# Kernel optimization log

Hardware: AMD Instinct MI355X
Metric: run time of the kernel (lower is better)

## Reference

```python
import jax, jax.numpy as jnp
import numpy as np

B, S, D, H, DK, DV, SEG = 2, 4096, 1024, 8, 128, 128, 512
NSEG = S // SEG


def setup_inputs() -> dict:
    key = jax.random.key(0)
    k0, k1, k2, k3, k4, k5 = jax.random.split(key, 6)
    return {
        "x": jax.random.normal(k0, (B, S, D), jnp.float32),
        "Wk": jax.random.normal(k1, (H, D, DK), jnp.float32) / np.float32(np.sqrt(D)),
        "Wv": jax.random.normal(k2, (H, D, DV), jnp.float32) / np.float32(np.sqrt(D)),
        "Wq": jax.random.normal(k3, (H, D, DK), jnp.float32) / np.float32(np.sqrt(D)),
        "Wout": jax.random.normal(k4, (H * DV, D), jnp.float32) / np.float32(np.sqrt(H * DV)),
        "betas": jax.random.normal(k5, (1, H, 1, DV), jnp.float32),
    }


def reference(x, Wk, Wv, Wq, Wout, betas):
    # Per-head projections: (B,H,S,dk/dv)
    k_full = jnp.einsum('bsd,hdk->bhsk', x, Wk)
    v_full = jnp.einsum('bsd,hdk->bhsk', x, Wv)
    q_full = jnp.einsum('bsd,hdk->bhsk', x, Wq)

    def to_segs(t):  # (B,H,S,E) -> (NSEG,B,H,SEG,E)
        return t.reshape(B, H, NSEG, SEG, t.shape[-1]).transpose(2, 0, 1, 3, 4)

    segs = (to_segs(k_full), to_segs(v_full), to_segs(q_full))

    mem0 = jnp.zeros((B, H, DK, DV), x.dtype)           # compressive memory
    z0 = jnp.full((B, H, DK, 1), 1.0 / DK, x.dtype)     # normalizer
    causal_mask = jnp.tril(jnp.ones((SEG, SEG), bool))
    gate = jax.nn.sigmoid(betas)                        # (1,H,1,DV)
    scale = jnp.asarray(1.0 / np.sqrt(DK), x.dtype)

    def step(carry, seg):
        mem, z = carry
        k, v, q = seg                                   # (B,H,SEG,dk/dv)
        sigma_q = jax.nn.elu(q) + 1.0
        # segment-local causal softmax attention
        scores = jnp.einsum('bhik,bhjk->bhij', q, k) * scale
        scores = jnp.where(causal_mask, scores, -jnp.inf)
        att_dot = jax.nn.softmax(scores, axis=-1) @ v
        # linear-attention read from memory
        att_mem = (sigma_q @ mem) / (sigma_q @ z)
        # delta-rule memory update
        sigma_k = jax.nn.elu(k) + 1.0
        mem = mem + jnp.einsum('bhsk,bhsv->bhkv', sigma_k, v - (sigma_k @ mem) / (sigma_k @ z))
        z = z + jnp.sum(sigma_k, axis=-2, keepdims=True).swapaxes(-1, -2)
        # gated mix of memory and local attention
        att = gate * att_mem + (1.0 - gate) * att_dot   # (B,H,SEG,DV)
        att = att.transpose(0, 2, 1, 3).reshape(B, SEG, H * DV)
        return (mem, z), att @ Wout                     # (B,SEG,D)

    _, outs = jax.lax.scan(step, (mem0, z0), segs)      # (NSEG,B,SEG,D)
    return outs.transpose(1, 0, 2, 3).reshape(B, S, D)
```

## Files before the change

### kernel.cpp

```cpp
#include <hip/hip_runtime.h>

#define B_  2
#define S_  4096
#define D_  1024
#define H_  8
#define DK_ 128
#define DV_ 128
#define SEG_ 512
#define NSEG_ 8
#define BH_ 16
#define M_ 8192

typedef __attribute__((ext_vector_type(8))) short bf16x8;
typedef __attribute__((ext_vector_type(4))) float f32x4;

__device__ __forceinline__ float elu1(float x) { return x > 0.f ? x + 1.f : __expf(x); }
__device__ __forceinline__ float sigmoidf(float x) { return 1.f / (1.f + __expf(-x)); }

__device__ __forceinline__ unsigned short f2b(float f) {
    union { float f; unsigned int u; } x; x.f = f;
    unsigned int r = x.u + 0x7fffu + ((x.u >> 16) & 1u);
    return (unsigned short)(r >> 16);
}
__device__ __forceinline__ float b2f(unsigned short u) {
    union { unsigned int u; float f; } x; x.u = ((unsigned int)u) << 16; return x.f;
}

__device__ __forceinline__ void gl2lds16(const void* g, void* l) {
    __builtin_amdgcn_global_load_lds(
        (const __attribute__((address_space(1))) void*)g,
        (__attribute__((address_space(3))) void*)l, 16, 0, 0);
}

__global__ __launch_bounds__(256) void conv_bf16(
    const float* __restrict__ src, unsigned short* __restrict__ dst)
{
    int i = (blockIdx.x * 256 + threadIdx.x) * 4;
    float4 v = *(const float4*)(src + i);
    ushort4 o;
    o.x = f2b(v.x); o.y = f2b(v.y); o.z = f2b(v.z); o.w = f2b(v.w);
    *(ushort4*)(dst + i) = o;
}

__global__ __launch_bounds__(256) void transpose_conv(
    const float* __restrict__ src, unsigned short* __restrict__ dst, int R, int C)
{
    __shared__ float tile[32][33];
    const size_t moff = (size_t)blockIdx.z * R * C;
    src += moff; dst += moff;
    const int c0 = blockIdx.x * 32, r0 = blockIdx.y * 32;
    const int tx = threadIdx.x & 31, ty = threadIdx.x >> 5;
    #pragma unroll
    for (int i = 0; i < 32; i += 8)
        tile[ty + i][tx] = src[(size_t)(r0 + ty + i) * C + c0 + tx];
    __syncthreads();
    #pragma unroll
    for (int i = 0; i < 32; i += 8)
        dst[(size_t)(c0 + ty + i) * R + r0 + tx] = f2b(tile[tx][ty + i]);
}

__global__ __launch_bounds__(256) void transpose_conv3(
    const float* __restrict__ Wk, const float* __restrict__ Wv,
    const float* __restrict__ Wq, unsigned short* __restrict__ dst)
{
    __shared__ float tile[32][33];
    const int z = blockIdx.z;
    const int w = z >> 3;
    const float* src = (w == 0) ? Wk : (w == 1) ? Wv : Wq;
    src += (size_t)(z & 7) * 131072;
    dst += (size_t)z * 131072;
    const int c0 = blockIdx.x * 32, r0 = blockIdx.y * 32;
    const int tx = threadIdx.x & 31, ty = threadIdx.x >> 5;
    #pragma unroll
    for (int i = 0; i < 32; i += 8)
        tile[ty + i][tx] = src[(size_t)(r0 + ty + i) * 128 + c0 + tx];
    __syncthreads();
    #pragma unroll
    for (int i = 0; i < 32; i += 8)
        dst[(size_t)(c0 + ty + i) * 1024 + r0 + tx] = f2b(tile[tx][ty + i]);
}

__global__ __launch_bounds__(256) void colsum_k(
    const unsigned short* __restrict__ Kbb, float* __restrict__ colsum)
{
    __shared__ float red[32][128];
    const int t = threadIdx.x;
    const int bh = blockIdx.x >> 3, seg = blockIdx.x & 7;
    const unsigned short* Kp = Kbb + ((size_t)bh * 4096 + seg * 512) * 128;
    const int rbase = t >> 3, c0 = (t & 7) * 16;
    float part[16] = {};
    for (int chunk = 0; chunk < 16; ++chunk) {
        const unsigned short* p = Kp + (size_t)(chunk * 32 + rbase) * 128 + c0;
        bf16x8 a = *(const bf16x8*)p;
        bf16x8 b = *(const bf16x8*)(p + 8);
        #pragma unroll
        for (int j = 0; j < 8; ++j) {
            part[j]     += elu1(b2f((unsigned short)a[j]));
            part[j + 8] += elu1(b2f((unsigned short)b[j]));
        }
    }
    #pragma unroll
    for (int j = 0; j < 16; ++j) red[rbase][c0 + j] = part[j];
    __syncthreads();
    if (t < 128) {
        float s = 0.f;
        #pragma unroll
        for (int r = 0; r < 32; ++r) s += red[r][t];
        colsum[(size_t)blockIdx.x * 128 + t] = s;
    }
}

__global__ __launch_bounds__(256) void den_z(
    const unsigned short* __restrict__ Kbb, const float* __restrict__ colsum,
    float* __restrict__ den, float* __restrict__ zseg)
{
    __shared__ float zs[128];
    const int t = threadIdx.x;
    const int bh = blockIdx.x >> 3, seg = blockIdx.x & 7;
    if (t < 128) {
        float z = 1.f / 128.f;
        for (int j = 0; j < seg; ++j) z += colsum[(size_t)(bh * 8 + j) * 128 + t];
        zs[t] = z;
        zseg[(size_t)blockIdx.x * 128 + t] = z;
    }
    __syncthreads();
    #pragma unroll
    for (int rr = 0; rr < 2; ++rr) {
        int s = t + rr * 256;
        const unsigned short* kp = Kbb + ((size_t)bh * 4096 + seg * 512 + s) * 128;
        float d = 0.f;
        #pragma unroll 4
        for (int f = 0; f < 16; ++f) {
            bf16x8 a = *(const bf16x8*)(kp + f * 8);
            #pragma unroll
            for (int j = 0; j < 8; ++j)
                d += elu1(b2f((unsigned short)a[j])) * zs[f * 8 + j];
        }
        den[(size_t)bh * 4096 + seg * 512 + s] = d;
    }
}

__global__ __launch_bounds__(256) void sigma_kT2(
    const unsigned short* __restrict__ Kbb, const float* __restrict__ den,
    unsigned short* __restrict__ SkT, unsigned short* __restrict__ SkTs)
{
    __shared__ float tile[32][33];
    __shared__ float rden[32];
    const int bh = blockIdx.z;
    const int s0 = blockIdx.x * 32, dk0 = blockIdx.y * 32;
    const int tx = threadIdx.x & 31, ty = threadIdx.x >> 5;
    if (threadIdx.x < 32) rden[threadIdx.x] = 1.f / den[(size_t)bh * 4096 + s0 + threadIdx.x];
    #pragma unroll
    for (int i = 0; i < 32; i += 8)
        tile[ty + i][tx] = elu1(b2f(Kbb[((size_t)bh * 4096 + s0 + ty + i) * 128 + dk0 + tx]));
    __syncthreads();
    #pragma unroll
    for (int i = 0; i < 32; i += 8) {
        float v = tile[tx][ty + i];
        size_t o = ((size_t)bh * 128 + dk0 + ty + i) * 4096 + s0 + tx;
        SkT[o]  = f2b(v);
        SkTs[o] = f2b(v * rden[tx]);
    }
}

__device__ __forceinline__ void mfma_gemm_128(
    const unsigned short* __restrict__ A, int lda,
    const unsigned short* __restrict__ Bt, int ldb, int K,
    unsigned short* As, unsigned short* Bs, f32x4 acc[4][4])
{
    const int tid = threadIdx.x;
    const int wave = tid >> 6, lane = tid & 63;
    const int r4 = lane >> 2;
    const int c4s = (((lane & 3) ^ ((lane >> 2) & 3)) * 8);
    const int lrow = lane & 15, lquad = lane >> 4;
    const int sl8 = (lquad ^ (lrow & 3)) * 8;
    const int wm = (wave >> 1) * 64, wn = (wave & 1) * 64;
    const int ar0 = wave * 32, ar1 = wave * 32 + 16;
    const int T = K >> 5;

    auto STAGE = [&](int t, int bufidx) {
        unsigned short* Ab = As + bufidx * 4096;
        unsigned short* Bb = Bs + bufidx * 4096;
        const int kk = t * 32;
        gl2lds16(A  + (size_t)(ar0 + r4) * lda + kk + c4s, Ab + ar0 * 32);
        gl2lds16(A  + (size_t)(ar1 + r4) * lda + kk + c4s, Ab + ar1 * 32);
        gl2lds16(Bt + (size_t)(ar0 + r4) * ldb + kk + c4s, Bb + ar0 * 32);
        gl2lds16(Bt + (size_t)(ar1 + r4) * ldb + kk + c4s, Bb + ar1 * 32);
    };

    STAGE(0, 0);
    STAGE(1, 1);
    int cur = 0;
    for (int t = 0; t < T; ++t) {
        if (t + 2 < T) {
            int nb = cur + 2; if (nb >= 3) nb -= 3;
            STAGE(t + 2, nb);
            asm volatile("s_waitcnt vmcnt(8)" ::: "memory");
        } else if (t + 1 < T) {
            asm volatile("s_waitcnt vmcnt(4)" ::: "memory");
        } else {
            asm volatile("s_waitcnt vmcnt(0)" ::: "memory");
        }
        __builtin_amdgcn_s_barrier();
        __builtin_amdgcn_sched_barrier(0);
        const unsigned short* Ac = As + cur * 4096;
        const unsigned short* Bc = Bs + cur * 4096;
        bf16x8 af[4], bfr[4];
        #pragma unroll
        for (int i = 0; i < 4; ++i)
            af[i] = *(const bf16x8*)(Ac + (wm + i * 16 + lrow) * 32 + sl8);
        #pragma unroll
        for (int j = 0; j < 4; ++j)
            bfr[j] = *(const bf16x8*)(Bc + (wn + j * 16 + lrow) * 32 + sl8);
        #pragma unroll
        for (int i = 0; i < 4; ++i)
            #pragma unroll
            for (int j = 0; j < 4; ++j)
                acc[i][j] = __builtin_amdgcn_mfma_f32_16x16x32_bf16(af[i], bfr[j], acc[i][j], 0, 0, 0);
        __builtin_amdgcn_s_barrier();
        __builtin_amdgcn_sched_barrier(0);
        cur += 1; if (cur >= 3) cur -= 3;
    }
}

__global__ __launch_bounds__(256) void gemm_qkv_mfma(
    const unsigned short* __restrict__ xb, const unsigned short* __restrict__ Wtb,
    unsigned short* __restrict__ Qbb, unsigned short* __restrict__ Kbb,
    unsigned short* __restrict__ Vtb)
{
    __shared__ unsigned short As[3 * 128 * 32];
    __shared__ unsigned short Bs[3 * 128 * 32];
    const int m0 = blockIdx.x * 128;
    const int panel = blockIdx.y;
    const int which = panel >> 3, h = panel & 7;
    f32x4 acc[4][4] = {};
    mfma_gemm_128(xb + (size_t)m0 * 1024, 1024,
                  Wtb + (size_t)panel * 128 * 1024, 1024, 1024, As, Bs, acc);
    const int tid = threadIdx.x, wave = tid >> 6, lane = tid & 63;
    const int lrow = lane & 15, lquad = lane >> 4;
    const int wm = (wave >> 1) * 64, wn = (wave & 1) * 64;
    if (which == 1) {
        #pragma unroll
        for (int i = 0; i < 4; ++i) {
            int mb = m0 + wm + i * 16 + lquad * 4;
            int bb = mb >> 12, sb = mb & 4095;
            int bh = bb * 8 + h;
            size_t vbase = ((size_t)bh * 8 + (sb >> 9)) * 128;
            #pragma unroll
            for (int j = 0; j < 4; ++j) {
                int col = wn + j * 16 + lrow;
                ushort4 o;
                o.x = f2b(acc[i][j][0]); o.y = f2b(acc[i][j][1]);
                o.z = f2b(acc[i][j][2]); o.w = f2b(acc[i][j][3]);
                *(ushort4*)(Vtb + ((vbase + col) * 512 + (sb & 511))) = o;
            }
        }
    } else {
        unsigned short* Dst = (which == 0) ? Kbb : Qbb;
        #pragma unroll
        for (int i = 0; i < 4; ++i)
            #pragma unroll
            for (int r = 0; r < 4; ++r) {
                int m = m0 + wm + i * 16 + lquad * 4 + r;
                int bb = m >> 12, s = m & 4095;
                int bh = bb * 8 + h;
                size_t rowbase = ((size_t)bh * 4096 + s) * 128;
                #pragma unroll
                for (int j = 0; j < 4; ++j)
                    Dst[rowbase + wn + j * 16 + lrow] = f2b(acc[i][j][r]);
            }
    }
}

__global__ __launch_bounds__(256) void gemm_out_mfma(
    const unsigned short* __restrict__ A, const unsigned short* __restrict__ Bt,
    float* __restrict__ C)
{
    __shared__ unsigned short As[3 * 128 * 32];
    __shared__ unsigned short Bs[3 * 128 * 32];
    const int m0 = blockIdx.x * 128, n0 = blockIdx.y * 128;
    f32x4 acc[4][4] = {};
    mfma_gemm_128(A + (size_t)m0 * 1024, 1024,
                  Bt + (size_t)n0 * 1024, 1024, 1024, As, Bs, acc);
    const int tid = threadIdx.x, wave = tid >> 6, lane = tid & 63;
    const int lrow = lane & 15, lquad = lane >> 4;
    const int wm = (wave >> 1) * 64, wn = (wave & 1) * 64;
    #pragma unroll
    for (int i = 0; i < 4; ++i)
        #pragma unroll
        for (int r = 0; r < 4; ++r) {
            int m = m0 + wm + i * 16 + lquad * 4 + r;
            #pragma unroll
            for (int j = 0; j < 4; ++j)
                C[(size_t)m * 1024 + n0 + wn + j * 16 + lrow] = acc[i][j][r];
        }
}

__global__ __launch_bounds__(256) void ac_gemm(
    const unsigned short* __restrict__ SkT, const unsigned short* __restrict__ SkTs,
    const unsigned short* __restrict__ Vtb,
    unsigned short* __restrict__ Emat, float* __restrict__ Cmat)
{
    __shared__ unsigned short As [3 * 128 * 32];
    __shared__ unsigned short Bs1[3 * 128 * 32];
    __shared__ unsigned short Bs2[3 * 128 * 32];
    const int bh = blockIdx.x >> 3, seg = blockIdx.x & 7;
    const unsigned short* Ap  = SkT  + (size_t)bh * 128 * 4096 + seg * 512;
    const unsigned short* B1p = SkTs + (size_t)bh * 128 * 4096 + seg * 512;
    const unsigned short* B2p = Vtb  + (size_t)blockIdx.x * 128 * 512;
    const int tid = threadIdx.x;
    const int wave = tid >> 6, lane = tid & 63;
    const int r4 = lane >> 2;
    const int c4s = (((lane & 3) ^ ((lane >> 2) & 3)) * 8);
    const int lrow = lane & 15, lquad = lane >> 4;
    const int sl8 = (lquad ^ (lrow & 3)) * 8;
    const int wm = (wave >> 1) * 64, wn = (wave & 1) * 64;
    const int ar0 = wave * 32, ar1 = wave * 32 + 16;
    f32x4 e[4][4] = {}, c[4][4] = {};

    auto STAGE = [&](int t, int bufidx) {
        unsigned short* Ab  = As  + bufidx * 4096;
        unsigned short* B1b = Bs1 + bufidx * 4096;
        unsigned short* B2b = Bs2 + bufidx * 4096;
        const int kk = t * 32;
        gl2lds16(Ap  + (size_t)(ar0 + r4) * 4096 + kk + c4s, Ab  + ar0 * 32);
        gl2lds16(Ap  + (size_t)(ar1 + r4) * 4096 + kk + c4s, Ab  + ar1 * 32);
        gl2lds16(B1p + (size_t)(ar0 + r4) * 4096 + kk + c4s, B1b + ar0 * 32);
        gl2lds16(B1p + (size_t)(ar1 + r4) * 4096 + kk + c4s, B1b + ar1 * 32);
        gl2lds16(B2p + (size_t)(ar0 + r4) * 512  + kk + c4s, B2b + ar0 * 32);
        gl2lds16(B2p + (size_t)(ar1 + r4) * 512  + kk + c4s, B2b + ar1 * 32);
    };

    STAGE(0, 0);
    STAGE(1, 1);
    int cur = 0;
    for (int t = 0; t < 16; ++t) {
        if (t + 2 < 16) {
            int nb = cur + 2; if (nb >= 3) nb -= 3;
            STAGE(t + 2, nb);
            asm volatile("s_waitcnt vmcnt(12)" ::: "memory");
        } else if (t + 1 < 16) {
            asm volatile("s_waitcnt vmcnt(6)" ::: "memory");
        } else {
            asm volatile("s_waitcnt vmcnt(0)" ::: "memory");
        }
        __builtin_amdgcn_s_barrier();
        __builtin_amdgcn_sched_barrier(0);
        const unsigned short* Ac  = As  + cur * 4096;
        const unsigned short* B1c = Bs1 + cur * 4096;
        const unsigned short* B2c = Bs2 + cur * 4096;
        bf16x8 af[4], b1[4], b2[4];
        #pragma unroll
        for (int i = 0; i < 4; ++i)
            af[i] = *(const bf16x8*)(Ac + (wm + i * 16 + lrow) * 32 + sl8);
        #pragma unroll
        for (int j = 0; j < 4; ++j) {
            b1[j] = *(const bf16x8*)(B1c + (wn + j * 16 + lrow) * 32 + sl8);
            b2[j] = *(const bf16x8*)(B2c + (wn + j * 16 + lrow) * 32 + sl8);
        }
        #pragma unroll
        for (int i = 0; i < 4; ++i)
            #pragma unroll
            for (int j = 0; j < 4; ++j) {
                e[i][j] = __builtin_amdgcn_mfma_f32_16x16x32_bf16(af[i], b1[j], e[i][j], 0, 0, 0);
                c[i][j] = __builtin_amdgcn_mfma_f32_16x16x32_bf16(af[i], b2[j], c[i][j], 0, 0, 0);
            }
        __builtin_amdgcn_s_barrier();
        __builtin_amdgcn_sched_barrier(0);
        cur += 1; if (cur >= 3) cur -= 3;
    }
    #pragma unroll
    for (int i = 0; i < 4; ++i)
        #pragma unroll
        for (int r = 0; r < 4; ++r) {
            int m = wm + i * 16 + lquad * 4 + r;
            #pragma unroll
            for (int j = 0; j < 4; ++j) {
                int nn = wn + j * 16 + lrow;
                size_t o = (size_t)blockIdx.x * 16384 + (size_t)m * 128 + nn;
                Emat[o] = f2b(-e[i][j][r]);
                Cmat[o] = c[i][j][r];
            }
        }
}

__global__ __launch_bounds__(512) void scan_step(
    const unsigned short* __restrict__ Emat, const float* __restrict__ Cmat,
    unsigned short* __restrict__ Memb)
{
    __shared__ unsigned short msh[128][136];
    const int t = threadIdx.x;
    const int wv = t >> 6, lane = t & 63;
    const int n16 = lane & 15, quad = lane >> 4;
    const int bh = blockIdx.x;
    f32x4 macc[8] = {};
    for (int seg = 0; seg < 8; ++seg) {
        unsigned short* gm = Memb + ((size_t)(bh * 8 + seg)) * 16384;
        #pragma unroll
        for (int vt = 0; vt < 8; ++vt) {
            ushort4 o;
            o.x = f2b(macc[vt][0]); o.y = f2b(macc[vt][1]);
            o.z = f2b(macc[vt][2]); o.w = f2b(macc[vt][3]);
            *(ushort4*)&msh[vt * 16 + n16][wv * 16 + quad * 4] = o;
            *(ushort4*)(gm + (size_t)(vt * 16 + n16) * 128 + wv * 16 + quad * 4) = o;
        }
        if (seg == 7) break;
        __syncthreads();
        const unsigned short* Ep = Emat + ((size_t)(bh * 8 + seg)) * 16384
                                 + (size_t)(wv * 16 + n16) * 128;
        bf16x8 ea[4];
        #pragma unroll
        for (int kf = 0; kf < 4; ++kf)
            ea[kf] = *(const bf16x8*)(Ep + kf * 32 + quad * 8);
        const float* Cp = Cmat + ((size_t)(bh * 8 + seg)) * 16384
                        + (size_t)(wv * 16 + quad * 4) * 128;
        #pragma unroll
        for (int vt = 0; vt < 8; ++vt)
            #pragma unroll
            for (int r = 0; r < 4; ++r)
                macc[vt][r] += Cp[(size_t)r * 128 + vt * 16 + n16];
        #pragma unroll
        for (int vt = 0; vt < 8; ++vt)
            #pragma unroll
            for (int kf = 0; kf < 4; ++kf) {
                bf16x8 bfr = *(const bf16x8*)&msh[vt * 16 + n16][kf * 32 + quad * 8];
                macc[vt] = __builtin_amdgcn_mfma_f32_16x16x32_bf16(ea[kf], bfr, macc[vt], 0, 0, 0);
            }
        __syncthreads();
    }
}

__global__ __launch_bounds__(256) void attn_out(
    const unsigned short* __restrict__ Qbb, const unsigned short* __restrict__ Kbb,
    const unsigned short* __restrict__ Vtb, const unsigned short* __restrict__ Memb,
    const float* __restrict__ zseg, const float* __restrict__ betas,
    unsigned short* __restrict__ Attb)
{
    __shared__ unsigned short Pl[4][32][72];
    const int tid = threadIdx.x, wave = tid >> 6, lane = tid & 63;
    const int n = lane & 15, quad = lane >> 4;
    const int bh = blockIdx.x >> 3, seg = blockIdx.x & 7;
    const int a = blockIdx.y;
    const int qt = (wave < 2) ? a : 7 - a;
    const int sp = (wave & 1) * 2;
    const int b = bh >> 3, h = bh & 7;
    const float scale2 = 0.12751744979f;
    const float FSH2 = 23.083120654f;

    const unsigned short* Qp = Qbb + ((size_t)bh * 4096 + seg * 512 + qt * 64 + sp * 16) * 128;
    const unsigned short* Kp = Kbb + ((size_t)bh * 4096 + seg * 512) * 128;
    const unsigned short* Vp = Vtb + ((size_t)bh * 8 + seg) * 128 * 512;

    bf16x8 aQ[2][4];
    #pragma unroll
    for (int s = 0; s < 2; ++s)
        #pragma unroll
        for (int kc = 0; kc < 4; ++kc)
            aQ[s][kc] = *(const bf16x8*)(Qp + (size_t)(s * 16 + n) * 128 + kc * 32 + quad * 8);

    f32x4 O[2][8] = {};
    float lpart[2][4] = {};

    for (int jt = 0; jt <= qt; ++jt) {
        f32x4 Sf[2][4] = {};
        #pragma unroll
        for (int kc = 0; kc < 4; ++kc) {
            bf16x8 bK[4];
            #pragma unroll
            for (int ns = 0; ns < 4; ++ns)
                bK[ns] = *(const bf16x8*)(Kp + (size_t)(jt * 64 + ns * 16 + n) * 128 + kc * 32 + quad * 8);
            #pragma unroll
            for (int ns = 0; ns < 4; ++ns) {
                Sf[0][ns] = __builtin_amdgcn_mfma_f32_16x16x32_bf16(aQ[0][kc], bK[ns], Sf[0][ns], 0, 0, 0);
                Sf[1][ns] = __builtin_amdgcn_mfma_f32_16x16x32_bf16(aQ[1][kc], bK[ns], Sf[1][ns], 0, 0, 0);
            }
        }
        const bool diag = (jt == qt);
        #pragma unroll
        for (int s = 0; s < 2; ++s)
            #pragma unroll
            for (int reg = 0; reg < 4; ++reg) {
                #pragma unroll
                for (int ns = 0; ns < 4; ++ns) {
                    float sv = Sf[s][ns][reg] * scale2 - FSH2;
                    if (diag) {
                        int grow = qt * 64 + (sp + s) * 16 + quad * 4 + reg;
                        int gcol = jt * 64 + ns * 16 + n;
                        if (gcol > grow) sv = -1e30f;
                    }
                    float p = exp2f(sv);
                    lpart[s][reg] += p;
                    Pl[wave][s * 16 + quad * 4 + reg][ns * 16 + n] = f2b(p);
                }
            }
        bf16x8 aP[2][2];
        #pragma unroll
        for (int s = 0; s < 2; ++s) {
            aP[s][0] = *(const bf16x8*)&Pl[wave][s * 16 + n][quad * 8];
            aP[s][1] = *(const bf16x8*)&Pl[wave][s * 16 + n][32 + quad * 8];
        }
        #pragma unroll
        for (int dvs = 0; dvs < 8; ++dvs) {
            bf16x8 bV0 = *(const bf16x8*)(Vp + (size_t)(dvs * 16 + n) * 512 + jt * 64 + quad * 8);
            bf16x8 bV1 = *(const bf16x8*)(Vp + (size_t)(dvs * 16 + n) * 512 + jt * 64 + 32 + quad * 8);
            O[0][dvs] = __builtin_amdgcn_mfma_f32_16x16x32_bf16(aP[0][0], bV0, O[0][dvs], 0, 0, 0);
            O[0][dvs] = __builtin_amdgcn_mfma_f32_16x16x32_bf16(aP[0][1], bV1, O[0][dvs], 0, 0, 0);
            O[1][dvs] = __builtin_amdgcn_mfma_f32_16x16x32_bf16(aP[1][0], bV0, O[1][dvs], 0, 0, 0);
            O[1][dvs] = __builtin_amdgcn_mfma_f32_16x16x32_bf16(aP[1][1], bV1, O[1][dvs], 0, 0, 0);
        }
    }
    const float* zp = zseg + (size_t)(bh * 8 + seg) * 128;
    const unsigned short* Mp = Memb + (size_t)(bh * 8 + seg) * 16384;
    #pragma unroll
    for (int s = 0; s < 2; ++s) {
        float l_i[4];
        #pragma unroll
        for (int r = 0; r < 4; ++r) {
            float rs = lpart[s][r];
            rs += __shfl_xor(rs, 1);
            rs += __shfl_xor(rs, 2);
            rs += __shfl_xor(rs, 4);
            rs += __shfl_xor(rs, 8);
            l_i[r] = rs;
        }
        float den = 0.f;
        bf16x8 aS[4];
        #pragma unroll
        for (int kc = 0; kc < 4; ++kc) {
            float4 z0 = *(const float4*)(zp + kc * 32 + quad * 8);
            float4 z1 = *(const float4*)(zp + kc * 32 + quad * 8 + 4);
            float zv[8] = {z0.x, z0.y, z0.z, z0.w, z1.x, z1.y, z1.z, z1.w};
            bf16x8 aa;
            #pragma unroll
            for (int j = 0; j < 8; ++j) {
                float sv = elu1(b2f((unsigned short)aQ[s][kc][j]));
                den += sv * zv[j];
                aa[j] = (short)f2b(sv);
            }
            aS[kc] = aa;
        }
        den += __shfl_xor(den, 16);
        den += __shfl_xor(den, 32);
        f32x4 Om[8] = {};
        #pragma unroll
        for (int dvs = 0; dvs < 8; ++dvs)
            #pragma unroll
            for (int kc = 0; kc < 4; ++kc) {
                bf16x8 bm = *(const bf16x8*)(Mp + (size_t)(dvs * 16 + n) * 128 + kc * 32 + quad * 8);
                Om[dvs] = __builtin_amdgcn_mfma_f32_16x16x32_bf16(aS[kc], bm, Om[dvs], 0, 0, 0);
            }
        float irm[4], inv[4];
        #pragma unroll
        for (int r = 0; r < 4; ++r) {
            irm[r] = 1.f / __shfl(den, quad * 4 + r);
            inv[r] = 1.f / l_i[r];
        }
        #pragma unroll
        for (int dvs = 0; dvs < 8; ++dvs) {
            int dv = dvs * 16 + n;
            float g = sigmoidf(betas[h * 128 + dv]);
            #pragma unroll
            for (int r = 0; r < 4; ++r) {
                int srow = seg * 512 + qt * 64 + (sp + s) * 16 + quad * 4 + r;
                float val = g * Om[dvs][r] * irm[r] + (1.f - g) * O[s][dvs][r] * inv[r];
                Attb[((size_t)b * 4096 + srow) * 1024 + h * 128 + dv] = f2b(val);
            }
        }
    }
}

extern "C" void kernel_launch(void* const* d_in, const int* in_sizes, int n_in,
                              void* d_out, int out_size, void* d_ws, size_t ws_size,
                              hipStream_t stream) {
    const float* x     = (const float*)d_in[0];
    const float* Wk    = (const float*)d_in[1];
    const float* Wv    = (const float*)d_in[2];
    const float* Wq    = (const float*)d_in[3];
    const float* Wout  = (const float*)d_in[4];
    const float* betas = (const float*)d_in[5];
    float* out = (float*)d_out;

    unsigned short* Qbb  = (unsigned short*)d_ws;
    unsigned short* Kbb  = Qbb + 8388608;
    unsigned short* Vtb  = Kbb + 8388608;
    unsigned short* SkT  = Vtb + 8388608;
    unsigned short* SkTs = SkT + 8388608;
    unsigned short* Emat = SkTs + 8388608;
    unsigned short* Memb = Emat + 2097152;
    float* Cmat   = (float*)(Memb + 2097152);
    float* colsum = Cmat + 2097152;
    float* zseg   = colsum + 16384;
    float* den    = zseg + 16384;
    unsigned short* xb    = SkT;
    unsigned short* Wtb   = SkTs;
    unsigned short* Attb  = SkT;
    unsigned short* Woutb = SkTs;

    conv_bf16<<<8192, 256, 0, stream>>>(x, xb);
    transpose_conv3<<<dim3(4, 32, 24), 256, 0, stream>>>(Wk, Wv, Wq, Wtb);
    gemm_qkv_mfma<<<dim3(64, 24), 256, 0, stream>>>(xb, Wtb, Qbb, Kbb, Vtb);
    colsum_k<<<128, 256, 0, stream>>>(Kbb, colsum);
    den_z<<<128, 256, 0, stream>>>(Kbb, colsum, den, zseg);
    sigma_kT2<<<dim3(128, 4, 16), 256, 0, stream>>>(Kbb, den, SkT, SkTs);
    ac_gemm<<<128, 256, 0, stream>>>(SkT, SkTs, Vtb, Emat, Cmat);
    scan_step<<<16, 512, 0, stream>>>(Emat, Cmat, Memb);
    attn_out<<<dim3(128, 4), 256, 0, stream>>>(Qbb, Kbb, Vtb, Memb, zseg, betas, Attb);
    transpose_conv<<<dim3(32, 32, 1), 256, 0, stream>>>(Wout, Woutb, 1024, 1024);
    gemm_out_mfma<<<dim3(64, 8), 256, 0, stream>>>(Attb, Woutb, out);
}
```

Measured before the change: 358.9 us.

## Widen QKV projection GEMM tile to 128x256 with 512-thread blocks

```diff
diff --git a/kernel.cpp b/kernel.cpp
--- a/kernel.cpp
+++ b/kernel.cpp
@@ -223,22 +223,84 @@
     }
 }
 
-__global__ __launch_bounds__(256) void gemm_qkv_mfma(
+__device__ __forceinline__ void mfma_gemm_128x256(
+    const unsigned short* __restrict__ A, int lda,
+    const unsigned short* __restrict__ Bt, int ldb, int K,
+    unsigned short* As, unsigned short* Bs, f32x4 acc[4][4])
+{
+    const int tid = threadIdx.x;
+    const int wave = tid >> 6, lane = tid & 63;
+    const int r4 = lane >> 2;
+    const int c4s = (((lane & 3) ^ ((lane >> 2) & 3)) * 8);
+    const int lrow = lane & 15, lquad = lane >> 4;
+    const int sl8 = (lquad ^ (lrow & 3)) * 8;
+    const int wm = (wave >> 2) * 64, wn = (wave & 3) * 64;
+    const int ara  = wave * 16;
+    const int arb0 = wave * 32, arb1 = wave * 32 + 16;
+    const int T = K >> 5;
+
+    auto STAGE = [&](int t, int bufidx) {
+        unsigned short* Ab = As + bufidx * 4096;
+        unsigned short* Bb = Bs + bufidx * 8192;
+        const int kk = t * 32;
+        gl2lds16(A  + (size_t)(ara  + r4) * lda + kk + c4s, Ab + ara  * 32);
+        gl2lds16(Bt + (size_t)(arb0 + r4) * ldb + kk + c4s, Bb + arb0 * 32);
+        gl2lds16(Bt + (size_t)(arb1 + r4) * ldb + kk + c4s, Bb + arb1 * 32);
+    };
+
+    STAGE(0, 0);
+    STAGE(1, 1);
+    int cur = 0;
+    for (int t = 0; t < T; ++t) {
+        if (t + 2 < T) {
+            int nb = cur + 2; if (nb >= 3) nb -= 3;
+            STAGE(t + 2, nb);
+            asm volatile("s_waitcnt vmcnt(6)" ::: "memory");
+        } else if (t + 1 < T) {
+            asm volatile("s_waitcnt vmcnt(3)" ::: "memory");
+        } else {
+            asm volatile("s_waitcnt vmcnt(0)" ::: "memory");
+        }
+        __builtin_amdgcn_s_barrier();
+        __builtin_amdgcn_sched_barrier(0);
+        const unsigned short* Ac = As + cur * 4096;
+        const unsigned short* Bc = Bs + cur * 8192;
+        bf16x8 af[4], bfr[4];
+        #pragma unroll
+        for (int i = 0; i < 4; ++i)
+            af[i] = *(const bf16x8*)(Ac + (wm + i * 16 + lrow) * 32 + sl8);
+        #pragma unroll
+        for (int j = 0; j < 4; ++j)
+            bfr[j] = *(const bf16x8*)(Bc + (wn + j * 16 + lrow) * 32 + sl8);
+        #pragma unroll
+        for (int i = 0; i < 4; ++i)
+            #pragma unroll
+            for (int j = 0; j < 4; ++j)
+                acc[i][j] = __builtin_amdgcn_mfma_f32_16x16x32_bf16(af[i], bfr[j], acc[i][j], 0, 0, 0);
+        __builtin_amdgcn_s_barrier();
+        __builtin_amdgcn_sched_barrier(0);
+        cur += 1; if (cur >= 3) cur -= 3;
+    }
+}
+
+__global__ __launch_bounds__(512) void gemm_qkv_mfma(
     const unsigned short* __restrict__ xb, const unsigned short* __restrict__ Wtb,
     unsigned short* __restrict__ Qbb, unsigned short* __restrict__ Kbb,
     unsigned short* __restrict__ Vtb)
 {
     __shared__ unsigned short As[3 * 128 * 32];
-    __shared__ unsigned short Bs[3 * 128 * 32];
+    __shared__ unsigned short Bs[3 * 256 * 32];
     const int m0 = blockIdx.x * 128;
-    const int panel = blockIdx.y;
-    const int which = panel >> 3, h = panel & 7;
+    const int n0 = blockIdx.y * 256;
     f32x4 acc[4][4] = {};
-    mfma_gemm_128(xb + (size_t)m0 * 1024, 1024,
-                  Wtb + (size_t)panel * 128 * 1024, 1024, 1024, As, Bs, acc);
+    mfma_gemm_128x256(xb + (size_t)m0 * 1024, 1024,
+                      Wtb + (size_t)n0 * 1024, 1024, 1024, As, Bs, acc);
     const int tid = threadIdx.x, wave = tid >> 6, lane = tid & 63;
     const int lrow = lane & 15, lquad = lane >> 4;
-    const int wm = (wave >> 1) * 64, wn = (wave & 1) * 64;
+    const int wm = (wave >> 2) * 64, wn = (wave & 3) * 64;
+    const int p = blockIdx.y * 2 + (wn >> 7);
+    const int which = p >> 3, h = p & 7;
+    const int coln = wn & 127;
     if (which == 1) {
         #pragma unroll
         for (int i = 0; i < 4; ++i) {
@@ -248,7 +310,7 @@
             size_t vbase = ((size_t)bh * 8 + (sb >> 9)) * 128;
             #pragma unroll
             for (int j = 0; j < 4; ++j) {
-                int col = wn + j * 16 + lrow;
+                int col = coln + j * 16 + lrow;
                 ushort4 o;
                 o.x = f2b(acc[i][j][0]); o.y = f2b(acc[i][j][1]);
                 o.z = f2b(acc[i][j][2]); o.w = f2b(acc[i][j][3]);
@@ -267,7 +329,7 @@
                 size_t rowbase = ((size_t)bh * 4096 + s) * 128;
                 #pragma unroll
                 for (int j = 0; j < 4; ++j)
-                    Dst[rowbase + wn + j * 16 + lrow] = f2b(acc[i][j][r]);
+                    Dst[rowbase + coln + j * 16 + lrow] = f2b(acc[i][j][r]);
             }
     }
 }
@@ -598,7 +660,7 @@
 
     conv_bf16<<<8192, 256, 0, stream>>>(x, xb);
     transpose_conv3<<<dim3(4, 32, 24), 256, 0, stream>>>(Wk, Wv, Wq, Wtb);
-    gemm_qkv_mfma<<<dim3(64, 24), 256, 0, stream>>>(xb, Wtb, Qbb, Kbb, Vtb);
+    gemm_qkv_mfma<<<dim3(64, 12), 512, 0, stream>>>(xb, Wtb, Qbb, Kbb, Vtb);
     colsum_k<<<128, 256, 0, stream>>>(Kbb, colsum);
     den_z<<<128, 256, 0, stream>>>(Kbb, colsum, den, zseg);
     sigma_kT2<<<dim3(128, 4, 16), 256, 0, stream>>>(Kbb, den, SkT, SkTs);
```

Result: slower. 372.5 us (+3.8%).
